# Performance work log

Hardware: AMD Instinct MI355X
Metric: run time of the kernel (lower is better)

Reference implementation:

```python
import jax, jax.numpy as jnp
import numpy as np

B, N, K, NB = 8, 4096, 16, 8
MAX_RADIUS = 10.0
OUT_MUL = 64  # irreps_out = '64x1o' -> output dim 64*3 = 192


def setup_inputs() -> dict:
    key = jax.random.key(0)
    k1, k2 = jax.random.split(key)
    coords = jax.random.normal(k1, (B, N, 3), dtype=jnp.float32)
    tp_weight = jax.random.normal(k2, (1, NB, OUT_MUL), dtype=jnp.float32)
    return {"coords": coords, "tp_weight": tp_weight}


def _knn_indices(coords, k):
    # coords: [B, N, 3] -> nbr idx [B, N, k] (no self loops), per-batch kNN
    n = coords.shape[1]
    d2 = jnp.sum((coords[:, :, None, :] - coords[:, None, :, :]) ** 2, axis=-1)  # [B,N,N]
    d2 = jnp.where(jnp.eye(n, dtype=bool)[None], jnp.inf, d2)
    _, idx = jax.lax.top_k(-d2, k)  # k nearest
    return idx


def reference(coords, tp_weight):
    nbr = _knn_indices(coords, K)                                # [B,N,K] int32
    nbr_coords = jax.vmap(lambda c, i: c[i])(coords, nbr)        # [B,N,K,3]
    r = nbr_coords - coords[:, :, None, :]                       # sender - receiver
    dist = jnp.linalg.norm(r, axis=-1, keepdims=True)            # [B,N,K,1]
    rhat = r / (dist + 1e-8)                                     # 1x1o input
    cutoff = jnp.clip(dist / MAX_RADIUS, 0.0, 1.0)
    # gaussian soft one-hot over [0,1] with NB centers
    centers = jnp.linspace(0.0, 1.0, NB, dtype=coords.dtype)
    sigma = 1.0 / NB
    g = jnp.exp(-((cutoff - centers) ** 2) / (2.0 * sigma * sigma))  # [B,N,K,NB]
    s = jnp.sum(g, axis=-1, keepdims=True)
    rb = g / jnp.where(s > 0, s, jnp.ones_like(s))               # 8x0e input
    # FullyConnectedTensorProduct 1x1o x NBx0e -> OUT_MULx1o (shared weights)
    # path normalization: 1/sqrt(mul_in1 * mul_in2) = 1/sqrt(NB)
    alpha = 1.0 / np.sqrt(1 * NB)
    W = tp_weight[0]                                             # [NB, OUT_MUL]
    edge_feat = alpha * jnp.einsum('vw,bnkv,bnkm->bnkwm', W, rb, rhat)  # [B,N,K,64,3]
    # exactly k incoming edges per receiver -> scatter_mean == mean over K
    agg = jnp.mean(edge_feat, axis=2).reshape(B, N, OUT_MUL * 3)  # [B,N,192]
    return agg
```

## Files before the change

kernel.cpp:

```cpp
#include <hip/hip_runtime.h>

typedef unsigned int u32;
typedef unsigned long long u64;
typedef float v2f __attribute__((ext_vector_type(2)));

#define NBATCH 8
#define NPTS   4096
#define NQTOT  (NBATCH * NPTS)
#define KNN    16
#define NBASIS 8
#define OUTM   64
#define NSPLIT 8
#define WIN    (NPTS / NSPLIT)
#define QPB    64
#define TKNN   (QPB * NSPLIT)
#define GRP    8
#define BUFCAP 64
#define BUFSTR 65

#define SENT 0x7f800000ffffffffull

__device__ __forceinline__ void ce(u64& x, u64& y) {
  u64 a = x, b = y;
  bool sw = b < a;
  x = sw ? b : a;
  y = sw ? a : b;
}

template <int N>
__device__ __forceinline__ void oems_sort(u64* a) {
#pragma unroll
  for (int p = 1; p < N; p <<= 1) {
#pragma unroll
    for (int k = p; k >= 1; k >>= 1) {
#pragma unroll
      for (int j = k & (p - 1); j + k < N; j += 2 * k) {
#pragma unroll
        for (int i = 0; i < k; ++i) {
          int lo = i + j, hi = i + j + k;
          if (hi < N && (lo / (2 * p)) == (hi / (2 * p)))
            ce(a[lo], a[hi]);
        }
      }
    }
  }
}

__device__ __forceinline__ void merge16(u64 t[16], const u64 a[16]) {
  u64 m[16];
#pragma unroll
  for (int i = 0; i < 16; ++i) {
    u64 x = t[i], y = a[15 - i];
    m[i] = (x < y) ? x : y;
  }
#pragma unroll
  for (int k = 8; k >= 1; k >>= 1) {
#pragma unroll
    for (int i = 0; i < 16; ++i) {
      if ((i & k) == 0) ce(m[i], m[i | k]);
    }
  }
#pragma unroll
  for (int i = 0; i < 16; ++i) t[i] = m[i];
}

__device__ __forceinline__ v2f d2pair(v2f cx, v2f cy, v2f cz, v2f qx, v2f qy,
                                      v2f qz) {
#pragma clang fp contract(off)
  v2f dx = cx - qx;
  v2f dy = cy - qy;
  v2f dz = cz - qz;
  v2f d2 = (dx * dx + dy * dy) + dz * dz;
  return d2;
}

__global__ __launch_bounds__(TKNN, 4) void se3_kernel(
    const float* __restrict__ Xp, const float* __restrict__ Yp,
    const float* __restrict__ Zp, const float4* __restrict__ cpad,
    const float* __restrict__ Wmat, float* __restrict__ out) {
  __shared__ u64 sBuf[QPB * BUFSTR];
  __shared__ u32 sCnt[QPB];
  __shared__ float sThr[QPB];
  __shared__ float sM[QPB * 25];

  const int b = blockIdx.x;
  const int qg = blockIdx.y;
  const int tid = threadIdx.x;
  const int ql = tid & 63;
  const int sp = tid >> 6;
  const int qi = qg * QPB + ql;
  const int base = b * NPTS;

  if (tid < QPB) sCnt[tid] = 0;

  const float qx = Xp[base + qi];
  const float qy = Yp[base + qi];
  const float qz = Zp[base + qi];
  const v2f qxx = {qx, qx}, qyy = {qy, qy}, qzz = {qz, qz};

  const int wbase = __builtin_amdgcn_readfirstlane(sp * WIN);
  const v2f* xs2 = (const v2f*)(Xp + base + wbase);
  const v2f* ys2 = (const v2f*)(Yp + base + wbase);
  const v2f* zs2 = (const v2f*)(Zp + base + wbase);
  const int sj = qi - wbase;

  u64 t16[16];
  {
    float cd[16];
#pragma unroll
    for (int p = 0; p < 8; ++p) {
      v2f d2 = d2pair(xs2[p], ys2[p], zs2[p], qxx, qyy, qzz);
      cd[2 * p + 0] = d2.x;
      cd[2 * p + 1] = d2.y;
    }
#pragma unroll
    for (int i = 0; i < 16; ++i) {
      u64 v = ((u64)__float_as_uint(cd[i]) << 32) | (u32)(wbase + i);
      t16[i] = (i == sj) ? SENT : v;
    }
    oems_sort<16>(t16);
  }

  if (sp >= 1 && sp <= 4) {
#pragma unroll
    for (int e = 0; e < 16; ++e) sBuf[ql * BUFSTR + (sp - 1) * 16 + e] = t16[e];
  }
  __syncthreads();
  if (sp == 0) {
#pragma unroll
    for (int s = 0; s < 4; ++s) {
      u64 a[16];
#pragma unroll
      for (int e = 0; e < 16; ++e) a[e] = sBuf[ql * BUFSTR + s * 16 + e];
      merge16(t16, a);
    }
  }
  __syncthreads();
  if (sp >= 5) {
#pragma unroll
    for (int e = 0; e < 16; ++e) sBuf[ql * BUFSTR + (sp - 5) * 16 + e] = t16[e];
  }
  __syncthreads();
  if (sp == 0) {
#pragma unroll
    for (int s = 0; s < 3; ++s) {
      u64 a[16];
#pragma unroll
      for (int e = 0; e < 16; ++e) a[e] = sBuf[ql * BUFSTR + s * 16 + e];
      merge16(t16, a);
    }
    sThr[ql] = __uint_as_float((u32)(t16[15] >> 32));
  }
  __syncthreads();
  float thr = sThr[ql];

  const int selfgrp = (sj >= 0 && sj < WIN) ? (sj >> 3) : -1;
  const u32 selfbit = 1u << (sj & 7);

#pragma unroll
  for (int ph = 0; ph < 5; ++ph) {
    const int cstart = 16 << ph;
    const int cend = 32 << ph;
    for (int g = cstart; g < cend; g += GRP) {
      v2f d2p[4];
#pragma unroll
      for (int p = 0; p < 4; ++p)
        d2p[p] = d2pair(xs2[(g >> 1) + p], ys2[(g >> 1) + p],
                        zs2[(g >> 1) + p], qxx, qyy, qzz);
      u32 want = 0;
#pragma unroll
      for (int i = 0; i < GRP; ++i)
        want |= (d2p[i >> 1][i & 1] <= thr) ? (1u << i) : 0u;
      if ((g >> 3) == selfgrp) want &= ~selfbit;
      if (__any(want)) {
#pragma unroll
        for (int i = 0; i < GRP; ++i) {
          if (want & (1u << i)) {
            u32 slot = atomicAdd(&sCnt[ql], 1u);
            if (slot < BUFCAP)
              sBuf[ql * BUFSTR + slot] =
                  ((u64)__float_as_uint(d2p[i >> 1][i & 1]) << 32) |
                  (u32)(wbase + g + i);
          }
        }
      }
    }
    __syncthreads();
    if (sp == 0) {
      int n = (int)sCnt[ql];
      n = n < BUFCAP ? n : BUFCAP;
      for (int k = 0; __any(k < n); k += 16) {
        u64 a[16];
#pragma unroll
        for (int e = 0; e < 16; ++e)
          a[e] = (k + e < n) ? sBuf[ql * BUFSTR + k + e] : SENT;
        oems_sort<16>(a);
        merge16(t16, a);
      }
      sCnt[ql] = 0;
      sThr[ql] = __uint_as_float((u32)(t16[15] >> 32));
    }
    __syncthreads();
    thr = sThr[ql];
  }

  if (sp == 0) {
    float M[24];
#pragma unroll
    for (int j = 0; j < 24; ++j) M[j] = 0.f;
#pragma unroll
    for (int chk = 0; chk < 4; ++chk) {
      float4 nc[4];
      float dd[4];
#pragma unroll
      for (int e = 0; e < 4; ++e) {
        u64 v = t16[chk * 4 + e];
        nc[e] = cpad[base + (int)(u32)v];
        dd[e] = __uint_as_float((u32)(v >> 32));
      }
#pragma unroll
      for (int e = 0; e < 4; ++e) {
        float rx = nc[e].x - qx;
        float ry = nc[e].y - qy;
        float rz = nc[e].z - qz;
        float dist = sqrtf(dd[e]);
        float inv = 1.0f / (dist + 1e-8f);
        rx *= inv; ry *= inv; rz *= inv;
        float cut = fminf(dist * 0.1f, 1.0f);
        float g[NBASIS], s = 0.f;
#pragma unroll
        for (int v = 0; v < NBASIS; ++v) {
          float t = cut - (float)v * (1.0f / 7.0f);
          g[v] = __expf(-32.0f * t * t);
          s += g[v];
        }
        float rs = 1.0f / s;
#pragma unroll
        for (int v = 0; v < NBASIS; ++v) {
          float rb = g[v] * rs;
          M[v * 3 + 0] = fmaf(rb, rx, M[v * 3 + 0]);
          M[v * 3 + 1] = fmaf(rb, ry, M[v * 3 + 1]);
          M[v * 3 + 2] = fmaf(rb, rz, M[v * 3 + 2]);
        }
      }
    }
#pragma unroll
    for (int j = 0; j < 24; ++j) sM[ql * 25 + j] = M[j];
  }
  __syncthreads();

  float wreg[NBASIS];
#pragma unroll
  for (int v = 0; v < NBASIS; ++v) wreg[v] = Wmat[v * OUTM + ql];
  const float scale = 0.022097086912079608f;
#pragma unroll
  for (int i = 0; i < 8; ++i) {
    int q = sp * 8 + i;
    const float* mq = sM + q * 25;
    float a0 = 0.f, a1 = 0.f, a2 = 0.f;
#pragma unroll
    for (int v = 0; v < NBASIS; ++v) {
      a0 = fmaf(wreg[v], mq[v * 3 + 0], a0);
      a1 = fmaf(wreg[v], mq[v * 3 + 1], a1);
      a2 = fmaf(wreg[v], mq[v * 3 + 2], a2);
    }
    size_t o = (size_t)(base + qg * QPB + q) * (OUTM * 3) + ql * 3;
    out[o + 0] = a0 * scale;
    out[o + 1] = a1 * scale;
    out[o + 2] = a2 * scale;
  }
}

__global__ void prep_kernel(const float* __restrict__ coords,
                            float* __restrict__ Xp, float* __restrict__ Yp,
                            float* __restrict__ Zp, float4* __restrict__ cpad) {
  int i = blockIdx.x * 256 + threadIdx.x;
  if (i < NQTOT) {
    float x = coords[3 * i + 0];
    float y = coords[3 * i + 1];
    float z = coords[3 * i + 2];
    Xp[i] = x; Yp[i] = y; Zp[i] = z;
    cpad[i] = make_float4(x, y, z, 0.f);
  }
}

extern "C" void kernel_launch(void* const* d_in, const int* in_sizes, int n_in,
                              void* d_out, int out_size, void* d_ws, size_t ws_size,
                              hipStream_t stream) {
  const float* coords = (const float*)d_in[0];
  const float* Wmat = (const float*)d_in[1];
  float* out = (float*)d_out;

  char* w = (char*)d_ws;
  float* Xp = (float*)(w);
  float* Yp = (float*)(w + 131072);
  float* Zp = (float*)(w + 262144);
  float4* cpad = (float4*)(w + 393216);

  prep_kernel<<<dim3((NQTOT + 255) / 256), dim3(256), 0, stream>>>(coords, Xp, Yp, Zp, cpad);
  se3_kernel<<<dim3(NBATCH, NPTS / QPB), dim3(TKNN), 0, stream>>>(Xp, Yp, Zp, cpad, Wmat, out);
}
```

Measured before the change: 183.6 us.

## Keep running top-k in shared memory and spread merge and edge work across waves

The running top-16 list now lives in shared memory rather than in the registers of wave 0. This frees registers, and the launch-bounds occupancy hint is dropped. Each refinement phase's merge rotates to a different wave, and merges with no new candidates are skipped. Edge feature accumulation is split across four waves, each handling four neighbours, with a shared-memory reduction of the partial moments. This adds extra shared-memory traffic and a barrier in exchange for less serial work on a single wave.

```diff
diff --git a/kernel.cpp b/kernel.cpp
--- a/kernel.cpp
+++ b/kernel.cpp
@@ -16,7 +16,8 @@
 #define TKNN   (QPB * NSPLIT)
 #define GRP    8
 #define BUFCAP 64
-#define BUFSTR 65
+#define ROWSTR 81
+#define TOFF   64
 
 #define SENT 0x7f800000ffffffffull
 
@@ -74,11 +75,11 @@
   return d2;
 }
 
-__global__ __launch_bounds__(TKNN, 4) void se3_kernel(
+__global__ __launch_bounds__(TKNN) void se3_kernel(
     const float* __restrict__ Xp, const float* __restrict__ Yp,
     const float* __restrict__ Zp, const float4* __restrict__ cpad,
     const float* __restrict__ Wmat, float* __restrict__ out) {
-  __shared__ u64 sBuf[QPB * BUFSTR];
+  __shared__ u64 sBuf[QPB * ROWSTR];
   __shared__ u32 sCnt[QPB];
   __shared__ float sThr[QPB];
   __shared__ float sM[QPB * 25];
@@ -104,8 +105,8 @@
   const v2f* zs2 = (const v2f*)(Zp + base + wbase);
   const int sj = qi - wbase;
 
-  u64 t16[16];
   {
+    u64 s16[16];
     float cd[16];
 #pragma unroll
     for (int p = 0; p < 8; ++p) {
@@ -116,42 +117,54 @@
 #pragma unroll
     for (int i = 0; i < 16; ++i) {
       u64 v = ((u64)__float_as_uint(cd[i]) << 32) | (u32)(wbase + i);
-      t16[i] = (i == sj) ? SENT : v;
-    }
-    oems_sort<16>(t16);
-  }
-
-  if (sp >= 1 && sp <= 4) {
-#pragma unroll
-    for (int e = 0; e < 16; ++e) sBuf[ql * BUFSTR + (sp - 1) * 16 + e] = t16[e];
-  }
-  __syncthreads();
-  if (sp == 0) {
-#pragma unroll
-    for (int s = 0; s < 4; ++s) {
-      u64 a[16];
-#pragma unroll
-      for (int e = 0; e < 16; ++e) a[e] = sBuf[ql * BUFSTR + s * 16 + e];
-      merge16(t16, a);
-    }
-  }
-  __syncthreads();
-  if (sp >= 5) {
-#pragma unroll
-    for (int e = 0; e < 16; ++e) sBuf[ql * BUFSTR + (sp - 5) * 16 + e] = t16[e];
-  }
-  __syncthreads();
-  if (sp == 0) {
-#pragma unroll
-    for (int s = 0; s < 3; ++s) {
-      u64 a[16];
-#pragma unroll
-      for (int e = 0; e < 16; ++e) a[e] = sBuf[ql * BUFSTR + s * 16 + e];
-      merge16(t16, a);
-    }
-    sThr[ql] = __uint_as_float((u32)(t16[15] >> 32));
-  }
-  __syncthreads();
+      s16[i] = (i == sj) ? SENT : v;
+    }
+    oems_sort<16>(s16);
+
+    if (sp >= 1 && sp <= 4) {
+#pragma unroll
+      for (int e = 0; e < 16; ++e)
+        sBuf[ql * ROWSTR + (sp - 1) * 16 + e] = s16[e];
+    }
+    __syncthreads();
+    if (sp == 0) {
+      u64 t16[16];
+#pragma unroll
+      for (int e = 0; e < 16; ++e) t16[e] = s16[e];
+#pragma unroll
+      for (int s = 0; s < 4; ++s) {
+        u64 a[16];
+#pragma unroll
+        for (int e = 0; e < 16; ++e) a[e] = sBuf[ql * ROWSTR + s * 16 + e];
+        merge16(t16, a);
+      }
+#pragma unroll
+      for (int e = 0; e < 16; ++e) sBuf[ql * ROWSTR + TOFF + e] = t16[e];
+    }
+    __syncthreads();
+    if (sp >= 5) {
+#pragma unroll
+      for (int e = 0; e < 16; ++e)
+        sBuf[ql * ROWSTR + (sp - 5) * 16 + e] = s16[e];
+    }
+    __syncthreads();
+    if (sp == 0) {
+      u64 t16[16];
+#pragma unroll
+      for (int e = 0; e < 16; ++e) t16[e] = sBuf[ql * ROWSTR + TOFF + e];
+#pragma unroll
+      for (int s = 0; s < 3; ++s) {
+        u64 a[16];
+#pragma unroll
+        for (int e = 0; e < 16; ++e) a[e] = sBuf[ql * ROWSTR + s * 16 + e];
+        merge16(t16, a);
+      }
+#pragma unroll
+      for (int e = 0; e < 16; ++e) sBuf[ql * ROWSTR + TOFF + e] = t16[e];
+      sThr[ql] = __uint_as_float((u32)(t16[15] >> 32));
+    }
+    __syncthreads();
+  }
   float thr = sThr[ql];
 
   const int selfgrp = (sj >= 0 && sj < WIN) ? (sj >> 3) : -1;
@@ -178,7 +191,7 @@
           if (want & (1u << i)) {
             u32 slot = atomicAdd(&sCnt[ql], 1u);
             if (slot < BUFCAP)
-              sBuf[ql * BUFSTR + slot] =
+              sBuf[ql * ROWSTR + slot] =
                   ((u64)__float_as_uint(d2p[i >> 1][i & 1]) << 32) |
                   (u32)(wbase + g + i);
           }
@@ -186,66 +199,87 @@
       }
     }
     __syncthreads();
-    if (sp == 0) {
+    if (sp == ph + 1) {
       int n = (int)sCnt[ql];
       n = n < BUFCAP ? n : BUFCAP;
-      for (int k = 0; __any(k < n); k += 16) {
-        u64 a[16];
-#pragma unroll
-        for (int e = 0; e < 16; ++e)
-          a[e] = (k + e < n) ? sBuf[ql * BUFSTR + k + e] : SENT;
-        oems_sort<16>(a);
-        merge16(t16, a);
+      if (__any(n > 0)) {
+        u64 t16[16];
+#pragma unroll
+        for (int e = 0; e < 16; ++e) t16[e] = sBuf[ql * ROWSTR + TOFF + e];
+        for (int k = 0; __any(k < n); k += 16) {
+          u64 a[16];
+#pragma unroll
+          for (int e = 0; e < 16; ++e)
+            a[e] = (k + e < n) ? sBuf[ql * ROWSTR + k + e] : SENT;
+          oems_sort<16>(a);
+          merge16(t16, a);
+        }
+#pragma unroll
+        for (int e = 0; e < 16; ++e) sBuf[ql * ROWSTR + TOFF + e] = t16[e];
+        sThr[ql] = __uint_as_float((u32)(t16[15] >> 32));
       }
       sCnt[ql] = 0;
-      sThr[ql] = __uint_as_float((u32)(t16[15] >> 32));
     }
     __syncthreads();
     thr = sThr[ql];
   }
 
-  if (sp == 0) {
+  if (sp < 4) {
+    const int k = sp;
+    u64 pv[4];
+#pragma unroll
+    for (int e = 0; e < 4; ++e)
+      pv[e] = sBuf[ql * ROWSTR + TOFF + k * 4 + e];
+    float4 nc[4];
+    float dd[4];
+#pragma unroll
+    for (int e = 0; e < 4; ++e) {
+      nc[e] = cpad[base + (int)(u32)pv[e]];
+      dd[e] = __uint_as_float((u32)(pv[e] >> 32));
+    }
     float M[24];
 #pragma unroll
     for (int j = 0; j < 24; ++j) M[j] = 0.f;
 #pragma unroll
-    for (int chk = 0; chk < 4; ++chk) {
-      float4 nc[4];
-      float dd[4];
-#pragma unroll
-      for (int e = 0; e < 4; ++e) {
-        u64 v = t16[chk * 4 + e];
-        nc[e] = cpad[base + (int)(u32)v];
-        dd[e] = __uint_as_float((u32)(v >> 32));
-      }
-#pragma unroll
-      for (int e = 0; e < 4; ++e) {
-        float rx = nc[e].x - qx;
-        float ry = nc[e].y - qy;
-        float rz = nc[e].z - qz;
-        float dist = sqrtf(dd[e]);
-        float inv = 1.0f / (dist + 1e-8f);
-        rx *= inv; ry *= inv; rz *= inv;
-        float cut = fminf(dist * 0.1f, 1.0f);
-        float g[NBASIS], s = 0.f;
-#pragma unroll
-        for (int v = 0; v < NBASIS; ++v) {
-          float t = cut - (float)v * (1.0f / 7.0f);
-          g[v] = __expf(-32.0f * t * t);
-          s += g[v];
-        }
-        float rs = 1.0f / s;
-#pragma unroll
-        for (int v = 0; v < NBASIS; ++v) {
-          float rb = g[v] * rs;
-          M[v * 3 + 0] = fmaf(rb, rx, M[v * 3 + 0]);
-          M[v * 3 + 1] = fmaf(rb, ry, M[v * 3 + 1]);
-          M[v * 3 + 2] = fmaf(rb, rz, M[v * 3 + 2]);
-        }
-      }
-    }
-#pragma unroll
-    for (int j = 0; j < 24; ++j) sM[ql * 25 + j] = M[j];
+    for (int e = 0; e < 4; ++e) {
+      float rx = nc[e].x - qx;
+      float ry = nc[e].y - qy;
+      float rz = nc[e].z - qz;
+      float dist = sqrtf(dd[e]);
+      float inv = 1.0f / (dist + 1e-8f);
+      rx *= inv; ry *= inv; rz *= inv;
+      float cut = fminf(dist * 0.1f, 1.0f);
+      float g[NBASIS], s = 0.f;
+#pragma unroll
+      for (int v = 0; v < NBASIS; ++v) {
+        float t = cut - (float)v * (1.0f / 7.0f);
+        g[v] = __expf(-32.0f * t * t);
+        s += g[v];
+      }
+      float rs = 1.0f / s;
+#pragma unroll
+      for (int v = 0; v < NBASIS; ++v) {
+        float rb = g[v] * rs;
+        M[v * 3 + 0] = fmaf(rb, rx, M[v * 3 + 0]);
+        M[v * 3 + 1] = fmaf(rb, ry, M[v * 3 + 1]);
+        M[v * 3 + 2] = fmaf(rb, rz, M[v * 3 + 2]);
+      }
+    }
+    float* fp = (float*)(sBuf + ql * ROWSTR);
+#pragma unroll
+    for (int c = 0; c < 24; ++c) fp[k * 25 + c] = M[c];
+  }
+  __syncthreads();
+
+  {
+    const float* fp = (const float*)(sBuf + ql * ROWSTR);
+#pragma unroll
+    for (int j0 = 0; j0 < 3; ++j0) {
+      int j = sp * 3 + j0;
+      float s = fp[0 * 25 + j] + fp[1 * 25 + j] + fp[2 * 25 + j] +
+                fp[3 * 25 + j];
+      sM[ql * 25 + j] = s;
+    }
   }
   __syncthreads();
 
```

After: 179.4 us. -2.3%, faster.
